# Performance work log

Hardware: AMD Instinct MI355X
Metric: run time of the kernel (lower is better)

## Reference

```python
import jax, jax.numpy as jnp
import numpy as np
from jax.scipy.special import logsumexp

# Per-part vertex counts from the original module (vertexnum[1:])
VERTEXNUM = [45, 61, 43, 45, 92, 34, 41, 62, 44, 44, 58, 42, 40, 60, 41, 35, 64, 28, 50, 62]
OFFSETS = np.concatenate([[0], np.cumsum(VERTEXNUM)])  # 21 offsets, total 985
BATCH = 2048
TOTAL_V = int(OFFSETS[-1])  # 985

# geomloss SamplesLoss(loss='sinkhorn', p=2, blur=0.05):
#   cost C(x,y) = |x-y|^2 / 2, eps_final = blur^p = 0.0025,
#   eps-scaling annealing from ~diameter^2 down to blur^2 (scaling=0.5 -> x0.25 per step),
#   debiased divergence S = OT(x,y) - 0.5*OT(x,x) - 0.5*OT(y,y).
BLUR2 = 0.05 ** 2
DIAM2 = 64.0  # static diameter^2 estimate for unit-gaussian point clouds
_eps, EPS_LIST = DIAM2, []
while _eps > BLUR2:
    EPS_LIST.append(_eps)
    _eps *= 0.25
EPS_LIST.append(BLUR2)


def _sqdist(x, y):
    # x: [n,3], y: [m,3] -> 0.5*||x_i - y_j||^2, shape [n,m]
    x2 = jnp.sum(x * x, axis=-1)
    y2 = jnp.sum(y * y, axis=-1)
    return 0.5 * (x2[:, None] + y2[None, :] - 2.0 * (x @ y.T))


def _sinkhorn_div(x, y):
    # Debiased entropic OT (Sinkhorn divergence), uniform weights, symmetric log-domain updates.
    n, m = x.shape[0], y.shape[0]
    loga = -float(np.log(n))
    logb = -float(np.log(m))
    Cxy = _sqdist(x, y)
    Cxx = _sqdist(x, x)
    Cyy = _sqdist(y, y)
    f = jnp.zeros((n,), dtype=x.dtype)
    g = jnp.zeros((m,), dtype=x.dtype)
    px = jnp.zeros((n,), dtype=x.dtype)
    py = jnp.zeros((m,), dtype=x.dtype)
    for eps in EPS_LIST:
        ft = -eps * logsumexp((g[None, :] - Cxy) / eps + logb, axis=1)
        gt = -eps * logsumexp((f[:, None] - Cxy) / eps + loga, axis=0)
        f = 0.5 * (f + ft)
        g = 0.5 * (g + gt)
        px = 0.5 * (px - eps * logsumexp((px[None, :] - Cxx) / eps + loga, axis=1))
        py = 0.5 * (py - eps * logsumexp((py[None, :] - Cyy) / eps + logb, axis=1))
    # S = <a, f - px> + <b, g - py>  (uniform weights -> means)
    return jnp.mean(f - px) + jnp.mean(g - py)


def setup_inputs() -> dict:
    key = jax.random.key(0)
    k1, k2 = jax.random.split(key)
    predvert = jax.random.normal(k1, (BATCH, TOTAL_V, 3), dtype=jnp.float32)
    batch_pointclouds = jax.random.normal(k2, (BATCH, TOTAL_V, 3), dtype=jnp.float32)
    return {"predvert": predvert, "batch_pointclouds": batch_pointclouds}


def reference(predvert, batch_pointclouds):
    batch_size = predvert.shape[0]
    loss = jnp.asarray(0.0, dtype=predvert.dtype)
    for i in range(20):  # static loop over 20 structurally distinct parts
        s, e = int(OFFSETS[i]), int(OFFSETS[i + 1])
        xs = predvert[:, s:e, :]
        ys = batch_pointclouds[:, s:e, :]
        div = jax.vmap(_sinkhorn_div)(xs, ys)  # [B]
        loss = loss + jnp.sum(div) / batch_size
    return loss
```

## Files before the change

### kernel.cpp

```cpp
#include <hip/hip_runtime.h>
#include <math.h>

typedef float f32x2 __attribute__((ext_vector_type(2)));

#define NPARTS 20
#define BATCH  2048
#define TOTALV 991
#define NEPS   9

#define LOG2E 1.4426950408889634f
#define LN2   0.6931471805599453f

__constant__ int   c_start[NPARTS] = {0,45,106,149,194,286,320,361,423,467,511,569,611,651,711,752,787,851,879,929};
__constant__ int   c_n[NPARTS]     = {45,61,43,45,92,34,41,62,44,44,58,42,40,60,41,35,64,28,50,62};
__constant__ float c_eps[NEPS]     = {64.0f,16.0f,4.0f,1.0f,0.25f,0.0625f,0.015625f,0.00390625f,0.0025f};

__constant__ int c_w_np[4]       = {4,5,5,6};
__constant__ int c_w_part[4][6]  = {{4,7,19,15,0,0},{16,1,13,12,17,0},{10,18,0,3,8,0},{9,2,11,6,14,5}};
__constant__ int c_w_lane0[4][7] = {{0,23,39,55,64,64,64},{0,16,32,47,57,64,64},{0,15,28,40,52,63,64},{0,11,22,33,44,55,64}};
__constant__ int c_w_tb[4][6]    = {{0,92,154,216,0,0},{0,64,125,185,225,0},{0,58,108,153,198,0},{0,44,87,129,170,211}};

static __device__ __forceinline__ f32x2 sp(float v){ f32x2 r; r.x=v; r.y=v; return r; }
static __device__ __forceinline__ float gc(f32x2 v, int c){ return c ? v.y : v.x; }
static __device__ __forceinline__ f32x2 pexp2(f32x2 v){
    f32x2 r; r.x=__builtin_amdgcn_exp2f(v.x); r.y=__builtin_amdgcn_exp2f(v.y); return r;
}
#define PFMA(a,b,c) __builtin_elementwise_fma(a,b,c)
#define PMAX(a,b)   __builtin_elementwise_max(a,b)

__global__ __launch_bounds__(64) void sinkhorn_kernel(
    const float* __restrict__ pred, const float* __restrict__ pc,
    float* __restrict__ partial)
{
    __shared__ float4 sX[256];
    __shared__ float4 sY[256];
    __shared__ float2 sT[256];

    const int bid  = blockIdx.x;
    const int b    = bid >> 2;
    const int w    = bid & 3;
    const int lane = threadIdx.x;

    int pj = -1;
    const int np = c_w_np[w];
    #pragma unroll
    for (int j = 0; j < 6; ++j)
        if (j < np && lane >= c_w_lane0[w][j] && lane < c_w_lane0[w][j+1]) pj = j;
    const bool lact = (pj >= 0);
    const int jj   = lact ? pj : 0;
    const int part = c_w_part[w][jj];
    const int st   = c_start[part];
    const int n    = lact ? c_n[part] : 0;
    const int h    = (n + 3) >> 2;
    const int r0   = lact ? (lane - c_w_lane0[w][jj]) : 0;
    const int tb   = c_w_tb[w][jj];

    f32x2 X0[2],X1[2],X2[2],Y0[2],Y1[2],Y2[2];
    float xh[4], yh[4];
    bool ra[4];
    #pragma unroll
    for (int j=0;j<4;++j) {
        const int r = r0 + j*h;
        ra[j] = lact && (r < n);
        float a0=0.f,a1=0.f,a2=0.f,b0=0.f,b1=0.f,b2=0.f;
        if (ra[j]) {
            const float* xp = pred + ((size_t)b*TOTALV + st + r)*3;
            const float* yp = pc   + ((size_t)b*TOTALV + st + r)*3;
            a0=xp[0]; a1=xp[1]; a2=xp[2];
            b0=yp[0]; b1=yp[1]; b2=yp[2];
        }
        const int p=j>>1;
        if ((j&1)==0) { X0[p].x=a0; X1[p].x=a1; X2[p].x=a2; Y0[p].x=b0; Y1[p].x=b1; Y2[p].x=b2; }
        else          { X0[p].y=a0; X1[p].y=a1; X2[p].y=a2; Y0[p].y=b0; Y1[p].y=b1; Y2[p].y=b2; }
        xh[j] = -0.5f*(a0*a0+a1*a1+a2*a2);
        yh[j] = -0.5f*(b0*b0+b1*b1+b2*b2);
    }
    const float lA = lact ? -log2f((float)n) : 0.f;
    float f[4]={0,0,0,0}, g[4]={0,0,0,0}, px[4]={0,0,0,0}, py[4]={0,0,0,0};
    float ax[4], ay[4];

    for (int it=0; it<NEPS; ++it) {
        const float eps = c_eps[it];
        const float sc  = LOG2E/eps;
        const float ce  = -eps*LN2;
        #pragma unroll
        for (int j=0;j<4;++j) { ax[j]=xh[j]*sc; ay[j]=yh[j]*sc; }

        #pragma unroll
        for (int j=0;j<4;++j) if (ra[j]) {
            const int p=j>>1, c=j&1;
            const int tr = tb + r0 + j*h;
            sX[tr] = make_float4(gc(X0[p],c)*sc, gc(X1[p],c)*sc, gc(X2[p],c)*sc, fmaf(f[j],  sc, ax[j]+lA));
            sY[tr] = make_float4(gc(Y0[p],c)*sc, gc(Y1[p],c)*sc, gc(Y2[p],c)*sc, fmaf(g[j],  sc, ay[j]+lA));
            sT[tr] = make_float2(fmaf(px[j], sc, ax[j]+lA), fmaf(py[j], sc, ay[j]+lA));
        }

        f32x2 MF[2],MG[2],MP[2],MQ[2];
        #pragma unroll
        for (int p=0;p<2;++p){ MF[p]=sp(-INFINITY); MG[p]=sp(-INFINITY); MP[p]=sp(-INFINITY); MQ[p]=sp(-INFINITY); }

        float4 XA = sX[tb], YA = sY[tb]; float2 TT = sT[tb];
        for (int k=0; k<n; ++k) {
            const float4 XN = sX[tb+k+1];
            const float4 YN = sY[tb+k+1];
            const float2 TN = sT[tb+k+1];
            #pragma unroll
            for (int p=0;p<2;++p) {
                const f32x2 wf = PFMA(X0[p],sp(YA.x), PFMA(X1[p],sp(YA.y), PFMA(X2[p],sp(YA.z), sp(YA.w))));
                const f32x2 wq = PFMA(Y0[p],sp(YA.x), PFMA(Y1[p],sp(YA.y), PFMA(Y2[p],sp(YA.z), sp(TT.y))));
                const f32x2 wg = PFMA(Y0[p],sp(XA.x), PFMA(Y1[p],sp(XA.y), PFMA(Y2[p],sp(XA.z), sp(XA.w))));
                const f32x2 wp = PFMA(X0[p],sp(XA.x), PFMA(X1[p],sp(XA.y), PFMA(X2[p],sp(XA.z), sp(TT.x))));
                MF[p]=PMAX(MF[p],wf); MQ[p]=PMAX(MQ[p],wq);
                MG[p]=PMAX(MG[p],wg); MP[p]=PMAX(MP[p],wp);
            }
            XA=XN; YA=YN; TT=TN;
        }

        f32x2 SF[2],SG[2],SP[2],SQ[2];
        #pragma unroll
        for (int p=0;p<2;++p){ SF[p]=sp(0.f); SG[p]=sp(0.f); SP[p]=sp(0.f); SQ[p]=sp(0.f); }
        XA = sX[tb]; YA = sY[tb]; TT = sT[tb];
        for (int k=0; k<n; ++k) {
            const float4 XN = sX[tb+k+1];
            const float4 YN = sY[tb+k+1];
            const float2 TN = sT[tb+k+1];
            #pragma unroll
            for (int p=0;p<2;++p) {
                const f32x2 wf = PFMA(X0[p],sp(YA.x), PFMA(X1[p],sp(YA.y), PFMA(X2[p],sp(YA.z), sp(YA.w))));
                const f32x2 wq = PFMA(Y0[p],sp(YA.x), PFMA(Y1[p],sp(YA.y), PFMA(Y2[p],sp(YA.z), sp(TT.y))));
                const f32x2 wg = PFMA(Y0[p],sp(XA.x), PFMA(Y1[p],sp(XA.y), PFMA(Y2[p],sp(XA.z), sp(XA.w))));
                const f32x2 wp = PFMA(X0[p],sp(XA.x), PFMA(X1[p],sp(XA.y), PFMA(X2[p],sp(XA.z), sp(TT.x))));
                SF[p] += pexp2(wf - MF[p]);
                SQ[p] += pexp2(wq - MQ[p]);
                SG[p] += pexp2(wg - MG[p]);
                SP[p] += pexp2(wp - MP[p]);
            }
            XA=XN; YA=YN; TT=TN;
        }

        #pragma unroll
        for (int j=0;j<4;++j) {
            const int p=j>>1, c=j&1;
            f[j]  = 0.5f*(f[j]  + ce*(ax[j] + gc(MF[p],c) + __builtin_amdgcn_logf(gc(SF[p],c))));
            g[j]  = 0.5f*(g[j]  + ce*(ay[j] + gc(MG[p],c) + __builtin_amdgcn_logf(gc(SG[p],c))));
            px[j] = 0.5f*(px[j] + ce*(ax[j] + gc(MP[p],c) + __builtin_amdgcn_logf(gc(SP[p],c))));
            py[j] = 0.5f*(py[j] + ce*(ay[j] + gc(MQ[p],c) + __builtin_amdgcn_logf(gc(SQ[p],c))));
        }
    }

    float d = 0.f;
    #pragma unroll
    for (int j=0;j<4;++j) if (ra[j]) d += (f[j]-px[j]) + (g[j]-py[j]);
    if (lact) d *= 1.0f/(float)n;
    #pragma unroll
    for (int o=32;o>0;o>>=1) d += __shfl_down(d, o, 64);
    if (lane==0) partial[bid] = d * (1.0f/(float)BATCH);
}

__global__ __launch_bounds__(1024) void reduce_kernel(
    const float* __restrict__ partial, float* __restrict__ out, int nb)
{
    const int t = threadIdx.x;
    double acc = 0.0;
    for (int i=t; i<nb; i+=blockDim.x) acc += (double)partial[i];
    #pragma unroll
    for (int o=32; o>0; o>>=1) acc += __shfl_down(acc, o, 64);
    __shared__ double ws[16];
    if ((t & 63) == 0) ws[t >> 6] = acc;
    __syncthreads();
    if (t == 0) {
        double tot = 0.0;
        for (int v=0; v<1024/64; ++v) tot += ws[v];
        out[0] = (float)tot;
    }
}

extern "C" void kernel_launch(void* const* d_in, const int* in_sizes, int n_in,
                              void* d_out, int out_size, void* d_ws, size_t ws_size,
                              hipStream_t stream) {
    const float* pred = (const float*)d_in[0];
    const float* pc   = (const float*)d_in[1];
    float* partial = (float*)d_ws;
    float* out     = (float*)d_out;
    sinkhorn_kernel<<<BATCH*4, 64, 0, stream>>>(pred, pc, partial);
    reduce_kernel<<<1, 1024, 0, stream>>>(partial, out, BATCH*4);
}
```

Before: 1.467 ms.

## Pack two waves per block and hand-write packed FMA with op_sel broadcasts

Each block now holds two 64-lane waves that cover two of the four part groups of a batch item. The LDS layout is doubled and offset per wave, and the partial index is remapped to match. The inner distance computations use inline-asm v_pk_fma_f32 with op_sel to broadcast scalar components straight from the loaded vectors. This removes the separate splat moves and the software-prefetch rotation, and the loops are unrolled by two. The intent is fewer VALU instructions per pair and better CU packing, at the cost of opaque inline asm that limits compiler scheduling.

```diff
diff --git a/kernel.cpp b/kernel.cpp
--- a/kernel.cpp
+++ b/kernel.cpp
@@ -2,6 +2,7 @@
 #include <math.h>
 
 typedef float f32x2 __attribute__((ext_vector_type(2)));
+typedef float f32x4 __attribute__((ext_vector_type(4)));
 
 #define NPARTS 20
 #define BATCH  2048
@@ -20,26 +21,33 @@
 __constant__ int c_w_lane0[4][7] = {{0,23,39,55,64,64,64},{0,16,32,47,57,64,64},{0,15,28,40,52,63,64},{0,11,22,33,44,55,64}};
 __constant__ int c_w_tb[4][6]    = {{0,92,154,216,0,0},{0,64,125,185,225,0},{0,58,108,153,198,0},{0,44,87,129,170,211}};
 
+#define NROWS 496
+
 static __device__ __forceinline__ f32x2 sp(float v){ f32x2 r; r.x=v; r.y=v; return r; }
 static __device__ __forceinline__ float gc(f32x2 v, int c){ return c ? v.y : v.x; }
-static __device__ __forceinline__ f32x2 pexp2(f32x2 v){
-    f32x2 r; r.x=__builtin_amdgcn_exp2f(v.x); r.y=__builtin_amdgcn_exp2f(v.y); return r;
-}
-#define PFMA(a,b,c) __builtin_elementwise_fma(a,b,c)
-#define PMAX(a,b)   __builtin_elementwise_max(a,b)
 
-__global__ __launch_bounds__(64) void sinkhorn_kernel(
+#define PKF_LH(d,a,b,c) asm("v_pk_fma_f32 %0, %1, %2, %3 op_sel:[0,0,1] op_sel_hi:[1,0,1]" : "=v"(d) : "v"(a), "v"(b), "v"(c))
+#define PKF_LL(d,a,b,c) asm("v_pk_fma_f32 %0, %1, %2, %3 op_sel:[0,0,0] op_sel_hi:[1,0,0]" : "=v"(d) : "v"(a), "v"(b), "v"(c))
+#define PKF_HP(d,a,b,c) asm("v_pk_fma_f32 %0, %1, %2, %3 op_sel:[0,1,0] op_sel_hi:[1,1,1]" : "=v"(d) : "v"(a), "v"(b), "v"(c))
+#define PKF_LP(d,a,b,c) asm("v_pk_fma_f32 %0, %1, %2, %3 op_sel:[0,0,0] op_sel_hi:[1,0,1]" : "=v"(d) : "v"(a), "v"(b), "v"(c))
+#define PKSUB(d,w,m)    asm("v_pk_add_f32 %0, %1, %2 neg_lo:[0,1] neg_hi:[0,1]" : "=v"(d) : "v"(w), "v"(m))
+#define SMAX(m,w)       do { (m).x = fmaxf((m).x,(w).x); (m).y = fmaxf((m).y,(w).y); } while(0)
+
+__global__ __launch_bounds__(128) void sinkhorn_kernel(
     const float* __restrict__ pred, const float* __restrict__ pc,
     float* __restrict__ partial)
 {
-    __shared__ float4 sX[256];
-    __shared__ float4 sY[256];
-    __shared__ float2 sT[256];
+    __shared__ float4 sX[NROWS];
+    __shared__ float4 sY[NROWS];
+    __shared__ float2 sT[NROWS];
 
     const int bid  = blockIdx.x;
-    const int b    = bid >> 2;
-    const int w    = bid & 3;
-    const int lane = threadIdx.x;
+    const int b    = bid >> 1;
+    const int pair = bid & 1;
+    const int wv   = threadIdx.x >> 6;
+    const int lane = threadIdx.x & 63;
+    const int w    = pair ? (wv ? 2 : 1) : (wv ? 3 : 0);
+    const int rb   = wv ? (pair ? 253 : 251) : 0;
 
     int pj = -1;
     const int np = c_w_np[w];
@@ -53,7 +61,7 @@
     const int n    = lact ? c_n[part] : 0;
     const int h    = (n + 3) >> 2;
     const int r0   = lact ? (lane - c_w_lane0[w][jj]) : 0;
-    const int tb   = c_w_tb[w][jj];
+    const int tb   = rb + c_w_tb[w][jj];
 
     f32x2 X0[2],X1[2],X2[2],Y0[2],Y1[2],Y2[2];
     float xh[4], yh[4];
@@ -99,43 +107,44 @@
         #pragma unroll
         for (int p=0;p<2;++p){ MF[p]=sp(-INFINITY); MG[p]=sp(-INFINITY); MP[p]=sp(-INFINITY); MQ[p]=sp(-INFINITY); }
 
-        float4 XA = sX[tb], YA = sY[tb]; float2 TT = sT[tb];
+        #pragma unroll 2
         for (int k=0; k<n; ++k) {
-            const float4 XN = sX[tb+k+1];
-            const float4 YN = sY[tb+k+1];
-            const float2 TN = sT[tb+k+1];
+            const f32x4 XA = *reinterpret_cast<const f32x4*>(&sX[tb+k]);
+            const f32x4 YA = *reinterpret_cast<const f32x4*>(&sY[tb+k]);
+            const f32x2 TT = *reinterpret_cast<const f32x2*>(&sT[tb+k]);
+            const f32x2 XAxy = XA.xy, XAzw = XA.zw, YAxy = YA.xy, YAzw = YA.zw;
             #pragma unroll
             for (int p=0;p<2;++p) {
-                const f32x2 wf = PFMA(X0[p],sp(YA.x), PFMA(X1[p],sp(YA.y), PFMA(X2[p],sp(YA.z), sp(YA.w))));
-                const f32x2 wq = PFMA(Y0[p],sp(YA.x), PFMA(Y1[p],sp(YA.y), PFMA(Y2[p],sp(YA.z), sp(TT.y))));
-                const f32x2 wg = PFMA(Y0[p],sp(XA.x), PFMA(Y1[p],sp(XA.y), PFMA(Y2[p],sp(XA.z), sp(XA.w))));
-                const f32x2 wp = PFMA(X0[p],sp(XA.x), PFMA(X1[p],sp(XA.y), PFMA(X2[p],sp(XA.z), sp(TT.x))));
-                MF[p]=PMAX(MF[p],wf); MQ[p]=PMAX(MQ[p],wq);
-                MG[p]=PMAX(MG[p],wg); MP[p]=PMAX(MP[p],wp);
+                f32x2 wf,wq,wg,wp;
+                PKF_LH(wf, X2[p], YAzw, YAzw); PKF_HP(wf, X1[p], YAxy, wf); PKF_LP(wf, X0[p], YAxy, wf);
+                PKF_LH(wq, Y2[p], YAzw, TT  ); PKF_HP(wq, Y1[p], YAxy, wq); PKF_LP(wq, Y0[p], YAxy, wq);
+                PKF_LH(wg, Y2[p], XAzw, XAzw); PKF_HP(wg, Y1[p], XAxy, wg); PKF_LP(wg, Y0[p], XAxy, wg);
+                PKF_LL(wp, X2[p], XAzw, TT  ); PKF_HP(wp, X1[p], XAxy, wp); PKF_LP(wp, X0[p], XAxy, wp);
+                SMAX(MF[p], wf); SMAX(MQ[p], wq); SMAX(MG[p], wg); SMAX(MP[p], wp);
             }
-            XA=XN; YA=YN; TT=TN;
         }
 
         f32x2 SF[2],SG[2],SP[2],SQ[2];
         #pragma unroll
         for (int p=0;p<2;++p){ SF[p]=sp(0.f); SG[p]=sp(0.f); SP[p]=sp(0.f); SQ[p]=sp(0.f); }
-        XA = sX[tb]; YA = sY[tb]; TT = sT[tb];
+        #pragma unroll 2
         for (int k=0; k<n; ++k) {
-            const float4 XN = sX[tb+k+1];
-            const float4 YN = sY[tb+k+1];
-            const float2 TN = sT[tb+k+1];
+            const f32x4 XA = *reinterpret_cast<const f32x4*>(&sX[tb+k]);
+            const f32x4 YA = *reinterpret_cast<const f32x4*>(&sY[tb+k]);
+            const f32x2 TT = *reinterpret_cast<const f32x2*>(&sT[tb+k]);
+            const f32x2 XAxy = XA.xy, XAzw = XA.zw, YAxy = YA.xy, YAzw = YA.zw;
             #pragma unroll
             for (int p=0;p<2;++p) {
-                const f32x2 wf = PFMA(X0[p],sp(YA.x), PFMA(X1[p],sp(YA.y), PFMA(X2[p],sp(YA.z), sp(YA.w))));
-                const f32x2 wq = PFMA(Y0[p],sp(YA.x), PFMA(Y1[p],sp(YA.y), PFMA(Y2[p],sp(YA.z), sp(TT.y))));
-                const f32x2 wg = PFMA(Y0[p],sp(XA.x), PFMA(Y1[p],sp(XA.y), PFMA(Y2[p],sp(XA.z), sp(XA.w))));
-                const f32x2 wp = PFMA(X0[p],sp(XA.x), PFMA(X1[p],sp(XA.y), PFMA(X2[p],sp(XA.z), sp(TT.x))));
-                SF[p] += pexp2(wf - MF[p]);
-                SQ[p] += pexp2(wq - MQ[p]);
-                SG[p] += pexp2(wg - MG[p]);
-                SP[p] += pexp2(wp - MP[p]);
+                f32x2 wf,wq,wg,wp,d;
+                PKF_LH(wf, X2[p], YAzw, YAzw); PKF_HP(wf, X1[p], YAxy, wf); PKF_LP(wf, X0[p], YAxy, wf);
+                PKF_LH(wq, Y2[p], YAzw, TT  ); PKF_HP(wq, Y1[p], YAxy, wq); PKF_LP(wq, Y0[p], YAxy, wq);
+                PKF_LH(wg, Y2[p], XAzw, XAzw); PKF_HP(wg, Y1[p], XAxy, wg); PKF_LP(wg, Y0[p], XAxy, wg);
+                PKF_LL(wp, X2[p], XAzw, TT  ); PKF_HP(wp, X1[p], XAxy, wp); PKF_LP(wp, X0[p], XAxy, wp);
+                PKSUB(d, wf, MF[p]); SF[p].x += __builtin_amdgcn_exp2f(d.x); SF[p].y += __builtin_amdgcn_exp2f(d.y);
+                PKSUB(d, wq, MQ[p]); SQ[p].x += __builtin_amdgcn_exp2f(d.x); SQ[p].y += __builtin_amdgcn_exp2f(d.y);
+                PKSUB(d, wg, MG[p]); SG[p].x += __builtin_amdgcn_exp2f(d.x); SG[p].y += __builtin_amdgcn_exp2f(d.y);
+                PKSUB(d, wp, MP[p]); SP[p].x += __builtin_amdgcn_exp2f(d.x); SP[p].y += __builtin_amdgcn_exp2f(d.y);
             }
-            XA=XN; YA=YN; TT=TN;
         }
 
         #pragma unroll
@@ -154,7 +163,7 @@
     if (lact) d *= 1.0f/(float)n;
     #pragma unroll
     for (int o=32;o>0;o>>=1) d += __shfl_down(d, o, 64);
-    if (lane==0) partial[bid] = d * (1.0f/(float)BATCH);
+    if (lane==0) partial[(bid<<1)+wv] = d * (1.0f/(float)BATCH);
 }
 
 __global__ __launch_bounds__(1024) void reduce_kernel(
@@ -182,6 +191,6 @@
     const float* pc   = (const float*)d_in[1];
     float* partial = (float*)d_ws;
     float* out     = (float*)d_out;
-    sinkhorn_kernel<<<BATCH*4, 64, 0, stream>>>(pred, pc, partial);
+    sinkhorn_kernel<<<BATCH*2, 128, 0, stream>>>(pred, pc, partial);
     reduce_kernel<<<1, 1024, 0, stream>>>(partial, out, BATCH*4);
 }
```

New measurement: 1.649 ms. 12.4% more time.
